# Kernel optimization log

Hardware: AMD Instinct MI355X
Metric: run time of the kernel (lower is better)

The kernel has to match this reference:

```python
import jax, jax.numpy as jnp
import numpy as np

N_E = 8192
E_DIM = 256
LATENT = 768
OUT_DIM = 768
DECAY = 0.99
EPS = 1e-05
DEAD_THRESH = 0.05
RESET_CS = DEAD_THRESH * 1.2  # reset_cluster_size
RATIO = (8 * 2048) / N_E      # total_codes / n_e with world_size=1


def l2norm(t):
    return t / jnp.linalg.norm(t, axis=-1, keepdims=True)


def setup_inputs() -> dict:
    key = jax.random.key(0)
    ks = jax.random.split(key, 6)
    x = jax.random.normal(ks[0], (8, 2048, LATENT), dtype=jnp.float32)
    # project_in / project_out Linear params (torch Linear: y = x @ W.T + b)
    W_in = jax.random.normal(ks[1], (E_DIM, LATENT), dtype=jnp.float32) * (1.0 / np.sqrt(LATENT))
    b_in = jnp.zeros((E_DIM,), dtype=jnp.float32)
    W_out = jax.random.normal(ks[2], (OUT_DIM, E_DIM), dtype=jnp.float32) * (1.0 / np.sqrt(E_DIM))
    b_out = jnp.zeros((OUT_DIM,), dtype=jnp.float32)
    embed = jax.random.uniform(ks[3], (N_E, E_DIM), dtype=jnp.float32,
                               minval=-1.0 / N_E, maxval=1.0 / N_E)
    embed = l2norm(embed)
    embed_avg = embed
    cluster_size = jnp.ones((N_E,), dtype=jnp.float32) * RATIO  # after init_quantizer
    return {"x": x, "W_in": W_in, "b_in": b_in, "W_out": W_out, "b_out": b_out,
            "embed": embed, "embed_avg": embed_avg, "cluster_size": cluster_size}


def reference(x, W_in, b_in, W_out, b_out, embed, embed_avg, cluster_size):
    sg = jax.lax.stop_gradient
    x_proj = jnp.einsum('btl,el->bte', x, W_in) + b_in        # [B,T,e_dim]
    xf = x_proj.reshape(-1, E_DIM)                            # [n, e_dim]
    xn = l2norm(xf)
    embed_d = sg(embed)
    d = jnp.einsum('nd,cd->nc', xn, embed_d)                  # [n, n_e] similarity
    embed_ind = jnp.argmin(d, axis=1)                         # (faithful: argmin of dot)
    onehot = jax.nn.one_hot(embed_ind, N_E, dtype=jnp.float32)
    z_q = jnp.einsum('nc,cd->nd', onehot, embed_d)            # training path
    bins = onehot.sum(axis=0)                                 # [n_e]
    cluster_new = cluster_size * DECAY + bins * (1.0 - DECAY)
    embed_sum = jnp.einsum('nd,nc->cd', xn, onehot)
    embed_avg_new = embed_avg * DECAY + embed_sum * (1.0 - DECAY)
    # laplace smoothing * total
    total = cluster_new.sum()
    cs = (cluster_new + EPS) / (total + N_E * EPS) * total
    embed_norm = embed_avg_new / cs[:, None]
    # entropy losses on scaled distances
    p = jax.nn.softmax(d * 10.0, axis=-1)                     # [n, n_e]
    ap = p.mean(axis=0)
    entropy_to_max = -(ap * jnp.log(ap)).sum()
    entropy_to_min = (-(p * jnp.log(p)).sum(axis=-1)).mean()
    diversity_loss = -entropy_to_max
    commit_loss = jnp.mean((sg(z_q) - xn) ** 2)
    loss = 1.0 * commit_loss + 1.0 * diversity_loss
    # straight-through estimator
    z_q_st = xn + sg(z_q - xn)
    z_q_out = z_q_st.reshape(x_proj.shape)
    z_q_out = jnp.einsum('bte,oe->bto', z_q_out, W_out) + b_out
    # expire dead codes: replace with first k samples (masked, jit-friendly)
    expired = cluster_new < DEAD_THRESH * RATIO
    n = xn.shape[0]
    idx = jnp.clip(jnp.cumsum(expired.astype(jnp.int32)) - 1, 0, None) % n
    sampled = sg(xn)[idx]                                     # [n_e, e_dim]
    embed_final = jnp.where(expired[:, None], sampled, embed_norm)
    embed_avg_final = jnp.where(expired[:, None], sampled * (RESET_CS * RATIO), embed_avg_new)
    cluster_final = jnp.where(expired, RESET_CS * RATIO, cluster_new)
    return (z_q_out, embed_ind, loss, embed_final, embed_avg_final, cluster_final,
            entropy_to_min, commit_loss)
```

## Files before the change

kernel.cpp:

```cpp
#include <hip/hip_runtime.h>
#include <hip/hip_bf16.h>

typedef unsigned long long u64;
typedef __bf16 bf16_t;
typedef __attribute__((ext_vector_type(8))) __bf16 bf16x8;
typedef __attribute__((ext_vector_type(4))) __bf16 bf16x4;
typedef __attribute__((ext_vector_type(4))) float f32x4;

#define NROWS 16384
#define KLAT  768
#define EDIM  256
#define NE    8192
#define ODIM  768

#define OFF_ZQ   0
#define OFF_IND  12582912
#define OFF_LOSS 12599296
#define OFF_EMB  12599297
#define OFF_EAVG 14696449
#define OFF_CSF  16793601
#define OFF_EMIN 16801793
#define OFF_CMT  16801794

#define W_XN    0u
#define W_ESUM  16777216u
#define W_RMIN  25165824u
#define W_RZ    25296896u
#define W_RS1   25362432u
#define W_INVZ  25427968u
#define W_INDW  25493504u
#define W_BINS  25559040u
#define W_CN    25591808u
#define W_CSM   25624576u
#define W_IDXS  25657344u
#define W_AP    25690112u
#define W_SCAL  25722880u
#define W_END   25722896u

#define CANDCAP 16
#define PROWS   2048
#define PM      128
#define PN      128
#define PK      32

typedef __attribute__((address_space(3))) unsigned char lds_u8;
typedef __attribute__((address_space(1))) const unsigned char glb_u8;
static __device__ __forceinline__ void gload16(const void* g, void* l)
{
  __builtin_amdgcn_global_load_lds((glb_u8*)g, (lds_u8*)l, 16, 0, 0);
}

__global__ __launch_bounds__(256) void zero_out_kernel(float* __restrict__ out, int n)
{
  int i = blockIdx.x * 256 + threadIdx.x;
  if (i < n) out[i] = 0.0f;
}

__global__ __launch_bounds__(256) void gemm_in_kernel(
    const float* __restrict__ A, const float* __restrict__ B,
    const float* __restrict__ bias, float* __restrict__ C)
{
  __shared__ float As[16][68];
  __shared__ float Bs[16][68];
  const int tid = threadIdx.x;
  const int tx = tid & 15, ty = tid >> 4;
  const int bm = blockIdx.x << 6, bn = blockIdx.y << 6;
  const int lr = tid >> 2, lk = (tid & 3) << 2;
  const size_t aoff = (size_t)(bm + lr) * KLAT;
  const size_t boff = (size_t)(bn + lr) * KLAT;
  float acc[4][4] = {};
  for (int k0 = 0; k0 < KLAT; k0 += 16) {
    __syncthreads();
    float4 av = *(const float4*)(A + aoff + k0 + lk);
    float4 bv = *(const float4*)(B + boff + k0 + lk);
    As[lk + 0][lr] = av.x; As[lk + 1][lr] = av.y; As[lk + 2][lr] = av.z; As[lk + 3][lr] = av.w;
    Bs[lk + 0][lr] = bv.x; Bs[lk + 1][lr] = bv.y; Bs[lk + 2][lr] = bv.z; Bs[lk + 3][lr] = bv.w;
    __syncthreads();
#pragma unroll
    for (int kk = 0; kk < 16; ++kk) {
      float4 a4 = *(const float4*)&As[kk][ty << 2];
      float4 b4 = *(const float4*)&Bs[kk][tx << 2];
      float ar[4] = {a4.x, a4.y, a4.z, a4.w};
      float br[4] = {b4.x, b4.y, b4.z, b4.w};
#pragma unroll
      for (int i = 0; i < 4; ++i)
#pragma unroll
        for (int j = 0; j < 4; ++j)
          acc[i][j] = fmaf(ar[i], br[j], acc[i][j]);
    }
  }
  float4 b4 = *(const float4*)(bias + bn + (tx << 2));
  float bb[4] = {b4.x, b4.y, b4.z, b4.w};
#pragma unroll
  for (int i = 0; i < 4; ++i) {
    const size_t row = (size_t)(bm + (ty << 2) + i);
    float4 o = make_float4(acc[i][0] + bb[0], acc[i][1] + bb[1],
                           acc[i][2] + bb[2], acc[i][3] + bb[3]);
    *(float4*)(C + row * EDIM + bn + (tx << 2)) = o;
  }
}

__global__ __launch_bounds__(256) void l2norm_split_kernel(
    float* __restrict__ xnf, bf16_t* __restrict__ xh, bf16_t* __restrict__ xl)
{
  __shared__ float sb[4];
  const int r = blockIdx.x, t = threadIdx.x;
  const size_t o = (size_t)r * EDIM + t;
  float v = xnf[o];
  float s = v * v;
#pragma unroll
  for (int off = 32; off >= 1; off >>= 1) s += __shfl_xor(s, off);
  if ((t & 63) == 0) sb[t >> 6] = s;
  __syncthreads();
  float tot = sb[0] + sb[1] + sb[2] + sb[3];
  float nv = v / sqrtf(tot);
  xnf[o] = nv;
  bf16_t h = (bf16_t)nv;
  xh[o] = h;
  xl[o] = (bf16_t)(nv - (float)h);
}

__global__ __launch_bounds__(256) void split_kernel(
    const float* __restrict__ src, bf16_t* __restrict__ hi, bf16_t* __restrict__ lo)
{
  const int i = (blockIdx.x * 256 + threadIdx.x) << 2;
  float4 v = *(const float4*)(src + i);
  bf16_t h0 = (bf16_t)v.x, h1 = (bf16_t)v.y, h2 = (bf16_t)v.z, h3 = (bf16_t)v.w;
  bf16x4 hv = {h0, h1, h2, h3};
  bf16x4 lv = {(bf16_t)(v.x - (float)h0), (bf16_t)(v.y - (float)h1),
               (bf16_t)(v.z - (float)h2), (bf16_t)(v.w - (float)h3)};
  *(bf16x4*)(hi + i) = hv;
  *(bf16x4*)(lo + i) = lv;
}

__global__ __launch_bounds__(256) void phase1_mfma_kernel(
    const bf16_t* __restrict__ xh, const bf16_t* __restrict__ xl,
    const bf16_t* __restrict__ eh, const bf16_t* __restrict__ el,
    const int rowbase,
    u64* __restrict__ rowmin, float* __restrict__ rowZ, float* __restrict__ rowS1,
    bf16_t* __restrict__ P)
{
  __shared__ bf16_t Ab[PM * 64];
  __shared__ bf16_t Bb[PN * 64];
  const int tid  = threadIdx.x;
  const int lane = tid & 63;
  const int wave = tid >> 6;
  const int wm = wave >> 1, wn = wave & 1;
  const int brow = blockIdx.x * PM;
  const int bcol = blockIdx.y * PN;

  const int srow8 = lane >> 3;
  const int chunk = (lane & 7) ^ srow8;
  const bf16_t* gpa = (chunk & 4) ? xl : xh;
  const bf16_t* gpb = (chunk & 4) ? el : eh;
  const int within = (chunk & 3) << 3;
  const int acall0 = wave << 5;

  const bf16_t* ga0 = gpa + (size_t)(rowbase + brow + acall0 + srow8) * EDIM + within;
  const bf16_t* gb0 = gpb + (size_t)(bcol + acall0 + srow8) * EDIM + within;

  f32x4 acc[4][4] = {};

  for (int k0 = 0; k0 < EDIM; k0 += PK) {
    __syncthreads();
#pragma unroll
    for (int c = 0; c < 4; ++c) {
      const int rr = acall0 + (c << 3);
      gload16(ga0 + (size_t)(c << 3) * EDIM + k0, &Ab[rr * 64]);
      gload16(gb0 + (size_t)(c << 3) * EDIM + k0, &Bb[rr * 64]);
    }
    __syncthreads();

    const int swz = lane & 7;
    const int sh  = (lane >> 4) ^ swz;
    const int sl  = sh ^ 4;
    const int ar0 = (wm << 6) + (lane & 15);
    const int br0 = (wn << 6) + (lane & 15);
    bf16x8 bhf[4], blf[4];
#pragma unroll
    for (int n = 0; n < 4; ++n) {
      const int r = br0 + (n << 4);
      bhf[n] = *(const bf16x8*)&Bb[r * 64 + (sh << 3)];
      blf[n] = *(const bf16x8*)&Bb[r * 64 + (sl << 3)];
    }
#pragma unroll
    for (int m = 0; m < 4; ++m) {
      const int r = ar0 + (m << 4);
      bf16x8 ahf = *(const bf16x8*)&Ab[r * 64 + (sh << 3)];
      bf16x8 alf = *(const bf16x8*)&Ab[r * 64 + (sl << 3)];
#pragma unroll
      for (int n = 0; n < 4; ++n) {
        acc[m][n] = __builtin_amdgcn_mfma_f32_16x16x32_bf16(ahf, bhf[n], acc[m][n], 0, 0, 0);
        acc[m][n] = __builtin_amdgcn_mfma_f32_16x16x32_bf16(ahf, blf[n], acc[m][n], 0, 0, 0);
        acc[m][n] = __builtin_amdgcn_mfma_f32_16x16x32_bf16(alf, bhf[n], acc[m][n], 0, 0, 0);
      }
    }
  }

  const int colg  = bcol + (wn << 6) + (lane & 15);
  const int pbase = bcol + (wn << 6) + ((lane & 15) << 2);
  const int rl0   = brow + (wm << 6) + ((lane >> 4) << 2);
#pragma unroll
  for (int m = 0; m < 4; ++m) {
#pragma unroll
    for (int q = 0; q < 4; ++q) {
      const int rl = rl0 + (m << 4) + q;
      float Z = 0.f, S1 = 0.f;
      float dloc = 1e30f;
      int nbest = 0;
      bf16_t evv[4];
#pragma unroll
      for (int n = 0; n < 4; ++n) {
        float d = acc[m][n][q];
        float l = 10.f * d;
        float e = __expf(l);
        Z += e; S1 += l * e;
        evv[n] = (bf16_t)e;
        if (d < dloc) { dloc = d; nbest = n; }
      }
      bf16x4 pv = {evv[0], evv[1], evv[2], evv[3]};
      *(bf16x4*)(P + (size_t)rl * NE + pbase) = pv;
      float dmin = dloc;
#pragma unroll
      for (int off = 1; off < 16; off <<= 1) {
        dmin = fminf(dmin, __shfl_xor(dmin, off));
        Z  += __shfl_xor(Z, off);
        S1 += __shfl_xor(S1, off);
      }
      const int rg = rowbase + rl;
      if (dloc == dmin) {
        u64 key = ((u64)__float_as_uint(dloc + 2.0f) << 32)
                | (unsigned)(colg + (nbest << 4));
        atomicMin(rowmin + rg, key);
      }
      if ((lane & 15) == 0) {
        atomicAdd(rowZ + rg, Z);
        atomicAdd(rowS1 + rg, S1);
      }
    }
  }
}

__global__ __launch_bounds__(256) void colreduce_kernel(
    const bf16_t* __restrict__ P, const float* __restrict__ rowZ,
    const u64* __restrict__ rowmin, const int rowbase,
    float* __restrict__ ap, int* __restrict__ ccnt, int* __restrict__ clist)
{
  __shared__ float izs[64], ths[64];
  const int t = threadIdx.x;
  const int pc0 = blockIdx.x * 1024 + (t << 2);
  const int r0 = blockIdx.y * 64;
  if (t < 64) {
    const int rg = rowbase + r0 + t;
    izs[t] = 1.0f / rowZ[rg];
    float dmin = __uint_as_float((unsigned)(rowmin[rg] >> 32)) - 2.0f;
    ths[t] = __expf(10.f * (dmin + 3e-4f));
  }
  __syncthreads();
  const int Bbase = pc0 & ~63;
  const int sub   = (pc0 & 63) >> 2;
  float s0 = 0.f, s1 = 0.f, s2 = 0.f, s3 = 0.f;
  for (int r = 0; r < 64; ++r) {
    bf16x4 p4 = *(const bf16x4*)(P + (size_t)(r0 + r) * NE + pc0);
    float p0 = (float)p4[0], p1 = (float)p4[1], p2 = (float)p4[2], p3 = (float)p4[3];
    float iz = izs[r], th = ths[r];
    s0 = fmaf(p0, iz, s0); s1 = fmaf(p1, iz, s1);
    s2 = fmaf(p2, iz, s2); s3 = fmaf(p3, iz, s3);
    float pm = fminf(fminf(p0, p1), fminf(p2, p3));
    if (pm <= th) {
      const int rg = rowbase + r0 + r;
      float pvv[4] = {p0, p1, p2, p3};
      for (int n = 0; n < 4; ++n)
        if (pvv[n] <= th) {
          int pos = atomicAdd(ccnt + rg, 1);
          if (pos < CANDCAP) clist[(rg << 4) + pos] = Bbase + (n << 4) + sub;
        }
    }
  }
  atomicAdd(ap + pc0 + 0, s0); atomicAdd(ap + pc0 + 1, s1);
  atomicAdd(ap + pc0 + 2, s2); atomicAdd(ap + pc0 + 3, s3);
}

__global__ __launch_bounds__(256) void rowent_kernel(
    const float* __restrict__ rowZ, const float* __restrict__ rowS1,
    float* __restrict__ scal)
{
  __shared__ float sb[4];
  const int r = blockIdx.x * 256 + threadIdx.x;
  const int t = threadIdx.x;
  float Z = rowZ[r], S1 = rowS1[r];
  float ent = logf(Z) - S1 / Z;
#pragma unroll
  for (int off = 32; off >= 1; off >>= 1) ent += __shfl_xor(ent, off);
  if ((t & 63) == 0) sb[t >> 6] = ent;
  __syncthreads();
  if (t == 0) atomicAdd(scal + 1, sb[0] + sb[1] + sb[2] + sb[3]);
}

__global__ __launch_bounds__(256) void repair_kernel(
    const float* __restrict__ xnf, const float* __restrict__ embed,
    const u64* __restrict__ rowmin, const int* __restrict__ ccnt,
    const int* __restrict__ clist, int* __restrict__ indw,
    float* __restrict__ bins, int* __restrict__ binsI, float* __restrict__ out)
{
  const int t = threadIdx.x;
  const int row = blockIdx.x * 64 + (t >> 2);
  const int sub = t & 3;
  const int base = ((int)(unsigned)(rowmin[row] & 0xFFFFFFFFull)) & (NE - 1);
  int cnt = ccnt[row];
  if (cnt > CANDCAP) cnt = CANDCAP;
  float bestD = 1e30f;
  int bestI = NE;
  const float* xr = xnf + (size_t)row * EDIM + (sub << 6);
  for (int j = -1; j < cnt; ++j) {
    const int c = (j < 0) ? base : (clist[(row << 4) + j] & (NE - 1));
    const float* er = embed + (size_t)c * EDIM + (sub << 6);
    float s = 0.f;
#pragma unroll
    for (int k = 0; k < 64; k += 4) {
      float4 a = *(const float4*)(xr + k);
      float4 b = *(const float4*)(er + k);
      s = fmaf(a.x, b.x, s); s = fmaf(a.y, b.y, s);
      s = fmaf(a.z, b.z, s); s = fmaf(a.w, b.w, s);
    }
    s += __shfl_xor(s, 1);
    s += __shfl_xor(s, 2);
    if (s < bestD || (s == bestD && c < bestI)) { bestD = s; bestI = c; }
  }
  if (sub == 0) {
    indw[row] = bestI;
    out[OFF_IND + row] = (float)bestI;
    atomicAdd(bins + bestI, 1.0f);
    atomicAdd(binsI + bestI, 1);
  }
}

__global__ __launch_bounds__(256) void sortprep_kernel(
    const int* __restrict__ binsI, int* __restrict__ offs, int* __restrict__ cursor)
{
  __shared__ int ssum[256];
  const int t = threadIdx.x;
  const int base = t * 32;
  int loc[32];
  int cnt = 0;
#pragma unroll
  for (int j = 0; j < 32; ++j) { loc[j] = cnt; cnt += binsI[base + j]; }
  ssum[t] = cnt;
  __syncthreads();
  for (int off = 1; off < 256; off <<= 1) {
    int v = (t >= off) ? ssum[t - off] : 0;
    __syncthreads();
    ssum[t] += v;
    __syncthreads();
  }
  int run = (t > 0) ? ssum[t - 1] : 0;
#pragma unroll
  for (int j = 0; j < 32; ++j) {
    offs[base + j]   = run + loc[j];
    cursor[base + j] = run + loc[j];
  }
}

__global__ __launch_bounds__(256) void rowsort_kernel(
    const int* __restrict__ indw, int* __restrict__ cursor, int* __restrict__ sorted)
{
  const int r = blockIdx.x * 256 + threadIdx.x;
  const int ind = indw[r] & (NE - 1);
  int pos = atomicAdd(cursor + ind, 1);
  sorted[pos & (NROWS - 1)] = (ind << 14) | r;
}

__global__ __launch_bounds__(256) void esum_commit_kernel(
    const int* __restrict__ sorted, const int* __restrict__ offs,
    const int* __restrict__ binsI, const float* __restrict__ xnf,
    const float* __restrict__ embed, float* __restrict__ esum,
    float* __restrict__ scal)
{
  __shared__ int ent[64];
  __shared__ float sb[4];
  const int t = threadIdx.x;
  const int base = blockIdx.x * 64;
  if (t < 64) ent[t] = sorted[base + t];
  __syncthreads();
  float cm = 0.f;
  float acc = 0.f;
  int ccur = ent[0] >> 14;
#pragma unroll
  for (int j = 0; j < 64; ++j) {
    const int e = ent[j];
    const int c = e >> 14;
    const int r = e & (NROWS - 1);
    if (c != ccur) {
      const int s0 = offs[ccur], cn = binsI[ccur];
      float* ep = esum + (size_t)ccur * EDIM + t;
      if (s0 >= base && s0 + cn <= base + 64) *ep = acc;
      else atomicAdd(ep, acc);
      acc = 0.f;
      ccur = c;
    }
    float xv = xnf[(size_t)r * EDIM + t];
    acc += xv;
    float df = embed[(size_t)c * EDIM + t] - xv;
    cm = fmaf(df, df, cm);
  }
  {
    const int s0 = offs[ccur], cn = binsI[ccur];
    float* ep = esum + (size_t)ccur * EDIM + t;
    if (s0 >= base && s0 + cn <= base + 64) *ep = acc;
    else atomicAdd(ep, acc);
  }
#pragma unroll
  for (int off = 32; off >= 1; off >>= 1) cm += __shfl_xor(cm, off);
  if ((t & 63) == 0) sb[t >> 6] = cm;
  __syncthreads();
  if (t == 0) atomicAdd(scal + 2, sb[0] + sb[1] + sb[2] + sb[3]);
}

__global__ __launch_bounds__(256) void scalars_kernel(
    const float* __restrict__ ap, const float* __restrict__ scal, float* __restrict__ out)
{
  __shared__ float sb[4];
  const int t = threadIdx.x;
  float h = 0.f;
  for (int c = t; c < NE; c += 256) {
    float apv = ap[c] * (1.0f / NROWS);
    h -= apv * logf(apv);
  }
#pragma unroll
  for (int off = 32; off >= 1; off >>= 1) h += __shfl_xor(h, off);
  if ((t & 63) == 0) sb[t >> 6] = h;
  __syncthreads();
  if (t == 0) {
    float Hmax = sb[0] + sb[1] + sb[2] + sb[3];
    float commit = scal[2] * (1.0f / ((float)NROWS * (float)EDIM));
    float emin = scal[1] * (1.0f / (float)NROWS);
    out[OFF_LOSS] = commit - Hmax;
    out[OFF_EMIN] = emin;
    out[OFF_CMT]  = commit;
  }
}

__global__ __launch_bounds__(256) void cluster_kernel(
    const float* __restrict__ cs_in, const float* __restrict__ bins,
    float* __restrict__ cn, float* __restrict__ scal)
{
  __shared__ float sb[4];
  const int c = blockIdx.x * 256 + threadIdx.x;
  const int t = threadIdx.x;
  float v = cs_in[c] * 0.99f + bins[c] * 0.01f;
  cn[c] = v;
  float s = v;
#pragma unroll
  for (int off = 32; off >= 1; off >>= 1) s += __shfl_xor(s, off);
  if ((t & 63) == 0) sb[t >> 6] = s;
  __syncthreads();
  if (t == 0) atomicAdd(scal + 0, sb[0] + sb[1] + sb[2] + sb[3]);
}

__global__ __launch_bounds__(256) void scan_kernel(
    const float* __restrict__ cn, const float* __restrict__ scal,
    int* __restrict__ idxs, float* __restrict__ csm, float* __restrict__ out)
{
  __shared__ int ssum[256];
  const int t = threadIdx.x;
  const int base = t * 32;
  int cnt = 0;
  for (int j = 0; j < 32; ++j) cnt += (cn[base + j] < 0.1f) ? 1 : 0;
  ssum[t] = cnt;
  __syncthreads();
  for (int off = 1; off < 256; off <<= 1) {
    int v = (t >= off) ? ssum[t - off] : 0;
    __syncthreads();
    ssum[t] += v;
    __syncthreads();
  }
  int run = (t > 0) ? ssum[t - 1] : 0;
  const float total = scal[0];
  const float dscale = total / (total + (float)NE * 1e-5f);
  for (int j = 0; j < 32; ++j) {
    float v = cn[base + j];
    bool ex = v < 0.1f;
    run += ex ? 1 : 0;
    int idx = run - 1; if (idx < 0) idx = 0;
    idx &= (NROWS - 1);
    idxs[base + j] = idx;
    csm[base + j] = (v + 1e-5f) * dscale;
    out[OFF_CSF + base + j] = ex ? 0.12f : v;
  }
}

__global__ __launch_bounds__(256) void embed_out_kernel(
    const float* __restrict__ cn, const float* __restrict__ csm,
    const int* __restrict__ idxs, const float* __restrict__ xn,
    const float* __restrict__ embed_avg, const float* __restrict__ esum,
    float* __restrict__ out)
{
  const int c = blockIdx.x, t = threadIdx.x;
  float oe, oa;
  if (cn[c] < 0.1f) {
    float s = xn[(size_t)(idxs[c] & (NROWS - 1)) * EDIM + t];
    oe = s; oa = s * 0.12f;
  } else {
    float an = embed_avg[(size_t)c * EDIM + t] * 0.99f
             + esum[(size_t)c * EDIM + t] * 0.01f;
    oa = an; oe = an / csm[c];
  }
  out[OFF_EMB  + (size_t)c * EDIM + t] = oe;
  out[OFF_EAVG + (size_t)c * EDIM + t] = oa;
}

__global__ __launch_bounds__(256) void gemm_out_mfma_kernel(
    const bf16_t* __restrict__ eh, const bf16_t* __restrict__ el,
    const bf16_t* __restrict__ wh, const bf16_t* __restrict__ wl,
    const float* __restrict__ bias, const int* __restrict__ gather,
    float* __restrict__ C)
{
  __shared__ bf16_t Ab[PM * 64];
  __shared__ bf16_t Bb[PN * 64];
  const int tid  = threadIdx.x;
  const int lane = tid & 63;
  const int wave = tid >> 6;
  const int wm = wave >> 1, wn = wave & 1;
  const int bm   = blockIdx.x * PM;
  const int bcol = blockIdx.y * PN;

  const int srow8 = lane >> 3;
  const int chunk = (lane & 7) ^ srow8;
  const bf16_t* gpa = (chunk & 4) ? el : eh;
  const bf16_t* gpb = (chunk & 4) ? wl : wh;
  const int within = (chunk & 3) << 3;
  const int acall0 = wave << 5;

  const bf16_t* ga[4];
#pragma unroll
  for (int c = 0; c < 4; ++c) {
    const int gr = gather[bm + acall0 + (c << 3) + srow8] & (NE - 1);
    ga[c] = gpa + (size_t)gr * EDIM + within;
  }
  const bf16_t* gb0 = gpb + (size_t)(bcol + acall0 + srow8) * EDIM + within;

  f32x4 acc[4][4] = {};

  for (int k0 = 0; k0 < EDIM; k0 += PK) {
    __syncthreads();
#pragma unroll
    for (int c = 0; c < 4; ++c) {
      const int rr = acall0 + (c << 3);
      gload16(ga[c] + k0, &Ab[rr * 64]);
      gload16(gb0 + (size_t)(c << 3) * EDIM + k0, &Bb[rr * 64]);
    }
    __syncthreads();

    const int swz = lane & 7;
    const int sh  = (lane >> 4) ^ swz;
    const int sl  = sh ^ 4;
    const int ar0 = (wm << 6) + (lane & 15);
    const int br0 = (wn << 6) + (lane & 15);
    bf16x8 bhf[4], blf[4];
#pragma unroll
    for (int n = 0; n < 4; ++n) {
      const int r = br0 + (n << 4);
      bhf[n] = *(const bf16x8*)&Bb[r * 64 + (sh << 3)];
      blf[n] = *(const bf16x8*)&Bb[r * 64 + (sl << 3)];
    }
#pragma unroll
    for (int m = 0; m < 4; ++m) {
      const int r = ar0 + (m << 4);
      bf16x8 ahf = *(const bf16x8*)&Ab[r * 64 + (sh << 3)];
      bf16x8 alf = *(const bf16x8*)&Ab[r * 64 + (sl << 3)];
#pragma unroll
      for (int n = 0; n < 4; ++n) {
        acc[m][n] = __builtin_amdgcn_mfma_f32_16x16x32_bf16(ahf, bhf[n], acc[m][n], 0, 0, 0);
        acc[m][n] = __builtin_amdgcn_mfma_f32_16x16x32_bf16(ahf, blf[n], acc[m][n], 0, 0, 0);
        acc[m][n] = __builtin_amdgcn_mfma_f32_16x16x32_bf16(alf, bhf[n], acc[m][n], 0, 0, 0);
      }
    }
  }

  const int colb = bcol + (wn << 6) + (lane & 15);
  float bs[4];
#pragma unroll
  for (int n = 0; n < 4; ++n) bs[n] = bias[colb + (n << 4)];
  const int row0 = bm + (wm << 6) + ((lane >> 4) << 2);
#pragma unroll
  for (int m = 0; m < 4; ++m) {
#pragma unroll
    for (int q = 0; q < 4; ++q) {
      float* op = C + (size_t)(row0 + (m << 4) + q) * ODIM;
#pragma unroll
      for (int n = 0; n < 4; ++n)
        op[colb + (n << 4)] = acc[m][n][q] + bs[n];
    }
  }
}

extern "C" void kernel_launch(void* const* d_in, const int* in_sizes, int n_in,
                              void* d_out, int out_size, void* d_ws, size_t ws_size,
                              hipStream_t stream)
{
  const float* x         = (const float*)d_in[0];
  const float* W_in      = (const float*)d_in[1];
  const float* b_in      = (const float*)d_in[2];
  const float* W_out     = (const float*)d_in[3];
  const float* b_out     = (const float*)d_in[4];
  const float* embed     = (const float*)d_in[5];
  const float* embed_avg = (const float*)d_in[6];
  const float* cs_in     = (const float*)d_in[7];
  float* out = (float*)d_out;
  char* ws = (char*)d_ws;

  if (ws_size < (size_t)W_END) {
    zero_out_kernel<<<(out_size + 255) / 256, 256, 0, stream>>>(out, out_size);
    return;
  }

  bf16_t* xh = (bf16_t*)(ws + W_XN);
  bf16_t* xl = (bf16_t*)(ws + W_XN + 8388608u);
  bf16_t* eh = (bf16_t*)(ws + W_ESUM);
  bf16_t* el = (bf16_t*)(ws + W_ESUM + 4194304u);
  float*  esum = (float*)(ws + W_XN);
  bf16_t* wh   = (bf16_t*)(ws + W_XN + 8388608u);
  bf16_t* wl   = (bf16_t*)(ws + W_XN + 8388608u + 393216u);
  u64*   rowmin= (u64*)  (ws + W_RMIN);
  int*   offs  = (int*)  (ws + W_RMIN);
  int*   cursor= offs + NE;
  float* rowZ  = (float*)(ws + W_RZ);
  float* rowS1 = (float*)(ws + W_RS1);
  int*   binsI = (int*)  (ws + W_INVZ);
  int*   indw  = (int*)  (ws + W_INDW);
  float* bins  = (float*)(ws + W_BINS);
  float* cn    = (float*)(ws + W_CN);
  float* csm   = (float*)(ws + W_CSM);
  int*   idxs  = (int*)  (ws + W_IDXS);
  float* ap    = (float*)(ws + W_AP);
  float* scal  = (float*)(ws + W_SCAL);

  float*  xnf    = out + OFF_ZQ;
  bf16_t* Pbuf   = (bf16_t*)(out + OFF_ZQ + 4194304);
  int*    ccnt   = (int*)(out + OFF_EMB);
  int*    clist  = ccnt + NROWS;
  int*    sorted = clist + NROWS * CANDCAP;

  hipMemsetAsync(ws + W_RMIN, 0xFF, W_RZ - W_RMIN, stream);
  hipMemsetAsync(ws + W_RZ,   0,    W_END - W_RZ,  stream);
  hipMemsetAsync(ccnt, 0, NROWS * sizeof(int), stream);

  gemm_in_kernel<<<dim3(NROWS / 64, EDIM / 64), 256, 0, stream>>>(
      x, W_in, b_in, xnf);
  l2norm_split_kernel<<<NROWS, 256, 0, stream>>>(xnf, xh, xl);
  split_kernel<<<(NE * EDIM / 4) / 256, 256, 0, stream>>>(embed, eh, el);
  for (int p = 0; p < NROWS / PROWS; ++p) {
    const int rowbase = p * PROWS;
    phase1_mfma_kernel<<<dim3(PROWS / PM, NE / PN), 256, 0, stream>>>(
        xh, xl, eh, el, rowbase, rowmin, rowZ, rowS1, Pbuf);
    colreduce_kernel<<<dim3(NE / 1024, PROWS / 64), 256, 0, stream>>>(
        Pbuf, rowZ, rowmin, rowbase, ap, ccnt, clist);
  }
  hipMemsetAsync(ws + W_XN, 0, NE * EDIM * sizeof(float), stream);
  rowent_kernel<<<NROWS / 256, 256, 0, stream>>>(rowZ, rowS1, scal);
  repair_kernel<<<NROWS / 64, 256, 0, stream>>>(
      xnf, embed, rowmin, ccnt, clist, indw, bins, binsI, out);
  sortprep_kernel<<<1, 256, 0, stream>>>(binsI, offs, cursor);
  rowsort_kernel<<<NROWS / 256, 256, 0, stream>>>(indw, cursor, sorted);
  split_kernel<<<(ODIM * EDIM / 4) / 256, 256, 0, stream>>>(W_out, wh, wl);
  esum_commit_kernel<<<NROWS / 64, 256, 0, stream>>>(
      sorted, offs, binsI, xnf, embed, esum, scal);
  cluster_kernel<<<NE / 256, 256, 0, stream>>>(cs_in, bins, cn, scal);
  scan_kernel<<<1, 256, 0, stream>>>(cn, scal, idxs, csm, out);
  scalars_kernel<<<1, 256, 0, stream>>>(ap, scal, out);
  embed_out_kernel<<<NE, 256, 0, stream>>>(cn, csm, idxs, xnf, embed_avg, esum, out);
  gemm_out_mfma_kernel<<<dim3(NROWS / PM, ODIM / PN), 256, 0, stream>>>(
      eh, el, wh, wl, b_out, indw, out + OFF_ZQ);
}
```

Before: 1.016 ms.

## Replace FP32 input projection GEMM with 3-way bf16-split MFMA GEMM

The scalar FP32 FMA projection GEMM (x @ W_in^T) is replaced by an MFMA kernel. Both operands are split into high/mid/low bf16 parts and six cross-product MFMAs are accumulated to emulate FP32 accuracy. W_in is pre-split by a new kernel, and the activations are split on the fly while staging into LDS. The aim is to move this GEMM onto the matrix cores, at the cost of six MFMAs per tile, extra LDS traffic and a small accuracy difference from true FP32.

```diff
diff --git a/kernel.cpp b/kernel.cpp
--- a/kernel.cpp
+++ b/kernel.cpp
@@ -43,6 +43,11 @@
 #define PN      128
 #define PK      32
 
+#define GM 128
+#define GN 64
+#define GK 32
+#define ASTR 40
+
 typedef __attribute__((address_space(3))) unsigned char lds_u8;
 typedef __attribute__((address_space(1))) const unsigned char glb_u8;
 static __device__ __forceinline__ void gload16(const void* g, void* l)
@@ -56,47 +61,116 @@
   if (i < n) out[i] = 0.0f;
 }
 
-__global__ __launch_bounds__(256) void gemm_in_kernel(
-    const float* __restrict__ A, const float* __restrict__ B,
+__global__ __launch_bounds__(256) void split3_kernel(
+    const float* __restrict__ src, bf16_t* __restrict__ h3,
+    bf16_t* __restrict__ m3, bf16_t* __restrict__ l3)
+{
+  const int i = (blockIdx.x * 256 + threadIdx.x) << 2;
+  float4 v = *(const float4*)(src + i);
+  bf16_t hv[4], mv[4], lv[4];
+  float c[4] = {v.x, v.y, v.z, v.w};
+#pragma unroll
+  for (int j = 0; j < 4; ++j) {
+    bf16_t h = (bf16_t)c[j];
+    float r1 = c[j] - (float)h;
+    bf16_t m = (bf16_t)r1;
+    bf16_t l = (bf16_t)(r1 - (float)m);
+    hv[j] = h; mv[j] = m; lv[j] = l;
+  }
+  *(bf16x4*)(h3 + i) = *(bf16x4*)hv;
+  *(bf16x4*)(m3 + i) = *(bf16x4*)mv;
+  *(bf16x4*)(l3 + i) = *(bf16x4*)lv;
+}
+
+__global__ __launch_bounds__(256) void gemm_in_mfma_kernel(
+    const float* __restrict__ A,
+    const bf16_t* __restrict__ wh, const bf16_t* __restrict__ wm,
+    const bf16_t* __restrict__ wl,
     const float* __restrict__ bias, float* __restrict__ C)
 {
-  __shared__ float As[16][68];
-  __shared__ float Bs[16][68];
-  const int tid = threadIdx.x;
-  const int tx = tid & 15, ty = tid >> 4;
-  const int bm = blockIdx.x << 6, bn = blockIdx.y << 6;
-  const int lr = tid >> 2, lk = (tid & 3) << 2;
-  const size_t aoff = (size_t)(bm + lr) * KLAT;
-  const size_t boff = (size_t)(bn + lr) * KLAT;
-  float acc[4][4] = {};
-  for (int k0 = 0; k0 < KLAT; k0 += 16) {
-    __syncthreads();
-    float4 av = *(const float4*)(A + aoff + k0 + lk);
-    float4 bv = *(const float4*)(B + boff + k0 + lk);
-    As[lk + 0][lr] = av.x; As[lk + 1][lr] = av.y; As[lk + 2][lr] = av.z; As[lk + 3][lr] = av.w;
-    Bs[lk + 0][lr] = bv.x; Bs[lk + 1][lr] = bv.y; Bs[lk + 2][lr] = bv.z; Bs[lk + 3][lr] = bv.w;
-    __syncthreads();
-#pragma unroll
-    for (int kk = 0; kk < 16; ++kk) {
-      float4 a4 = *(const float4*)&As[kk][ty << 2];
-      float4 b4 = *(const float4*)&Bs[kk][tx << 2];
-      float ar[4] = {a4.x, a4.y, a4.z, a4.w};
-      float br[4] = {b4.x, b4.y, b4.z, b4.w};
-#pragma unroll
-      for (int i = 0; i < 4; ++i)
-#pragma unroll
-        for (int j = 0; j < 4; ++j)
-          acc[i][j] = fmaf(ar[i], br[j], acc[i][j]);
-    }
-  }
-  float4 b4 = *(const float4*)(bias + bn + (tx << 2));
-  float bb[4] = {b4.x, b4.y, b4.z, b4.w};
-#pragma unroll
-  for (int i = 0; i < 4; ++i) {
-    const size_t row = (size_t)(bm + (ty << 2) + i);
-    float4 o = make_float4(acc[i][0] + bb[0], acc[i][1] + bb[1],
-                           acc[i][2] + bb[2], acc[i][3] + bb[3]);
-    *(float4*)(C + row * EDIM + bn + (tx << 2)) = o;
+  __shared__ bf16_t Ah[GM * ASTR], Am[GM * ASTR], Al[GM * ASTR];
+  __shared__ bf16_t Bh[GN * ASTR], Bm[GN * ASTR], Bl[GN * ASTR];
+  const int tid  = threadIdx.x;
+  const int lane = tid & 63;
+  const int wave = tid >> 6;
+  const int wmr = wave >> 1, wnc = wave & 1;
+  const int bm = blockIdx.x * GM;
+  const int bn = blockIdx.y * GN;
+
+  const int brow = tid >> 2, bkc = tid & 3;
+
+  f32x4 acc[4][2] = {};
+
+  for (int k0 = 0; k0 < KLAT; k0 += GK) {
+    __syncthreads();
+#pragma unroll
+    for (int c = 0; c < 4; ++c) {
+      const int pos = (c << 8) + tid;
+      const int r = pos >> 3, kq = pos & 7;
+      float4 v = *(const float4*)(A + (size_t)(bm + r) * KLAT + k0 + (kq << 2));
+      float cc[4] = {v.x, v.y, v.z, v.w};
+      bf16_t hv[4], mv[4], lv[4];
+#pragma unroll
+      for (int j = 0; j < 4; ++j) {
+        bf16_t h = (bf16_t)cc[j];
+        float r1 = cc[j] - (float)h;
+        bf16_t m = (bf16_t)r1;
+        hv[j] = h; mv[j] = m; lv[j] = (bf16_t)(r1 - (float)m);
+      }
+      const int off = r * ASTR + (kq << 2);
+      *(bf16x4*)&Ah[off] = *(bf16x4*)hv;
+      *(bf16x4*)&Am[off] = *(bf16x4*)mv;
+      *(bf16x4*)&Al[off] = *(bf16x4*)lv;
+    }
+    {
+      const size_t g = (size_t)(bn + brow) * KLAT + k0 + (bkc << 3);
+      const int off = brow * ASTR + (bkc << 3);
+      *(bf16x8*)&Bh[off] = *(const bf16x8*)(wh + g);
+      *(bf16x8*)&Bm[off] = *(const bf16x8*)(wm + g);
+      *(bf16x8*)&Bl[off] = *(const bf16x8*)(wl + g);
+    }
+    __syncthreads();
+
+    const int koff = (lane >> 4) << 3;
+    const int br0 = (wnc << 5) + (lane & 15);
+    bf16x8 bh[2], bm2[2], bl2[2];
+#pragma unroll
+    for (int n = 0; n < 2; ++n) {
+      const int r = br0 + (n << 4);
+      bh[n]  = *(const bf16x8*)&Bh[r * ASTR + koff];
+      bm2[n] = *(const bf16x8*)&Bm[r * ASTR + koff];
+      bl2[n] = *(const bf16x8*)&Bl[r * ASTR + koff];
+    }
+    const int ar0 = (wmr << 6) + (lane & 15);
+#pragma unroll
+    for (int m = 0; m < 4; ++m) {
+      const int r = ar0 + (m << 4);
+      bf16x8 ah = *(const bf16x8*)&Ah[r * ASTR + koff];
+      bf16x8 am = *(const bf16x8*)&Am[r * ASTR + koff];
+      bf16x8 al = *(const bf16x8*)&Al[r * ASTR + koff];
+#pragma unroll
+      for (int n = 0; n < 2; ++n) {
+        acc[m][n] = __builtin_amdgcn_mfma_f32_16x16x32_bf16(ah, bh[n],  acc[m][n], 0, 0, 0);
+        acc[m][n] = __builtin_amdgcn_mfma_f32_16x16x32_bf16(ah, bm2[n], acc[m][n], 0, 0, 0);
+        acc[m][n] = __builtin_amdgcn_mfma_f32_16x16x32_bf16(am, bh[n],  acc[m][n], 0, 0, 0);
+        acc[m][n] = __builtin_amdgcn_mfma_f32_16x16x32_bf16(ah, bl2[n], acc[m][n], 0, 0, 0);
+        acc[m][n] = __builtin_amdgcn_mfma_f32_16x16x32_bf16(al, bh[n],  acc[m][n], 0, 0, 0);
+        acc[m][n] = __builtin_amdgcn_mfma_f32_16x16x32_bf16(am, bm2[n], acc[m][n], 0, 0, 0);
+      }
+    }
+  }
+
+  const int colb = bn + (wnc << 5) + (lane & 15);
+  const float bs0 = bias[colb], bs1 = bias[colb + 16];
+  const int row0 = bm + (wmr << 6) + ((lane >> 4) << 2);
+#pragma unroll
+  for (int m = 0; m < 4; ++m) {
+#pragma unroll
+    for (int q = 0; q < 4; ++q) {
+      float* op = C + (size_t)(row0 + (m << 4) + q) * EDIM;
+      op[colb]      = acc[m][0][q] + bs0;
+      op[colb + 16] = acc[m][1][q] + bs1;
+    }
   }
 }
 
@@ -614,6 +688,9 @@
     return;
   }
 
+  bf16_t* wih = (bf16_t*)(ws + W_XN);
+  bf16_t* wim = wih + (size_t)EDIM * KLAT;
+  bf16_t* wil = wim + (size_t)EDIM * KLAT;
   bf16_t* xh = (bf16_t*)(ws + W_XN);
   bf16_t* xl = (bf16_t*)(ws + W_XN + 8388608u);
   bf16_t* eh = (bf16_t*)(ws + W_ESUM);
@@ -645,8 +722,9 @@
   hipMemsetAsync(ws + W_RZ,   0,    W_END - W_RZ,  stream);
   hipMemsetAsync(ccnt, 0, NROWS * sizeof(int), stream);
 
-  gemm_in_kernel<<<dim3(NROWS / 64, EDIM / 64), 256, 0, stream>>>(
-      x, W_in, b_in, xnf);
+  split3_kernel<<<(EDIM * KLAT / 4) / 256, 256, 0, stream>>>(W_in, wih, wim, wil);
+  gemm_in_mfma_kernel<<<dim3(NROWS / GM, EDIM / GN), 256, 0, stream>>>(
+      x, wih, wim, wil, b_in, xnf);
   l2norm_split_kernel<<<NROWS, 256, 0, stream>>>(xnf, xh, xl);
   split_kernel<<<(NE * EDIM / 4) / 256, 256, 0, stream>>>(embed, eh, el);
   for (int p = 0; p < NROWS / PROWS; ++p) {
```

Result: faster. 985.8 us (-2.9%).
